# Optimization experiments

Measured on AMD Instinct MI355X. Metric: run time of the kernel, lower is better.

The kernel has to match this reference:

```python
import jax, jax.numpy as jnp
import numpy as np

B, S, HID = 2, 2048, 2048
NH, HD = 16, 128
KVC, QC = 512, 1536


def _rope(x):
    # x: [B, H, S, D]; interleaved-pair rotation matching the torch view(..., D//2, 2)
    b, h, s, d = x.shape
    inv_freq = 1.0 / (10000.0 ** (jnp.arange(0, d, 2, dtype=jnp.float32) / d))  # [D/2]
    pos = jnp.arange(s, dtype=jnp.float32)
    sinusoid = pos[:, None] * inv_freq[None, :]  # [S, D/2]
    sin = jnp.sin(sinusoid)[None, None]  # [1,1,S,D/2]
    cos = jnp.cos(sinusoid)[None, None]
    xr = x.reshape(b, h, s, d // 2, 2)
    x1, x2 = xr[..., 0], xr[..., 1]
    out = jnp.stack([x1 * cos - x2 * sin, x1 * sin + x2 * cos], axis=-1)
    return out.reshape(b, h, s, d)


def setup_inputs() -> dict:
    key = jax.random.key(0)
    ks = jax.random.split(key, 14)
    def lin(k, fan_in, fan_out):
        lim = 1.0 / np.sqrt(fan_in)
        kw, kb = jax.random.split(k)
        W = jax.random.uniform(kw, (fan_in, fan_out), jnp.float32, -lim, lim)
        b = jax.random.uniform(kb, (fan_out,), jnp.float32, -lim, lim)
        return W, b
    x = jax.random.normal(ks[0], (B, S, HID), jnp.float32)
    # causal mask (positions with 0 are masked out)
    attention_mask = jnp.tril(jnp.ones((S, S), jnp.int32))[None, None]  # [1,1,S,S]
    W_dkv, b_dkv = lin(ks[1], HID, KVC)
    W_uk, b_uk = lin(ks[2], KVC, NH * HD)
    W_uv, b_uv = lin(ks[3], KVC, NH * HD)
    W_dq, b_dq = lin(ks[4], HID, QC)
    W_uq, b_uq = lin(ks[5], QC, NH * HD)
    W_o, b_o = lin(ks[6], NH * HD, HID)
    return dict(x=x, attention_mask=attention_mask,
                W_dkv=W_dkv, b_dkv=b_dkv, W_uk=W_uk, b_uk=b_uk,
                W_uv=W_uv, b_uv=b_uv, W_dq=W_dq, b_dq=b_dq,
                W_uq=W_uq, b_uq=b_uq, W_o=W_o, b_o=b_o)


def reference(x, attention_mask, W_dkv, b_dkv, W_uk, b_uk, W_uv, b_uv,
              W_dq, b_dq, W_uq, b_uq, W_o, b_o):
    b, s, _ = x.shape
    kv = x @ W_dkv + b_dkv                                   # [B,S,KVC]
    k = (kv @ W_uk + b_uk).reshape(b, s, NH, HD).transpose(0, 2, 1, 3)  # [B,H,S,D]
    v = (kv @ W_uv + b_uv).reshape(b, s, NH, HD).transpose(0, 2, 1, 3)
    q = ((x @ W_dq + b_dq) @ W_uq + b_uq).reshape(b, s, NH, HD).transpose(0, 2, 1, 3)
    q, k = _rope(q), _rope(k)
    scores = jnp.einsum('bhqd,bhkd->bhqk', q, k) / jnp.sqrt(jnp.float32(HD))
    scores = jnp.where(attention_mask == 0, jnp.float32(-1e9), scores)
    probs = jax.nn.softmax(scores, axis=-1)
    out = jnp.einsum('bhqk,bhkd->bhqd', probs, v)            # [B,H,S,D]
    out = out.transpose(0, 2, 1, 3).reshape(b, s, NH * HD)
    return out @ W_o + b_o
```

## Files before the change

### kernel.cpp

```cpp
#include <hip/hip_runtime.h>
#include <stdint.h>

typedef unsigned short u16;
typedef uint32_t u32;
typedef __attribute__((ext_vector_type(8))) short short8;
typedef __attribute__((ext_vector_type(4))) float f32x4;
typedef __attribute__((ext_vector_type(4))) u32 u32x4;
typedef __attribute__((ext_vector_type(2))) u32 u32x2;
typedef __attribute__((ext_vector_type(4))) unsigned short u16x4;

#define BS_ 4096
#define S_ 2048
#define HID_ 2048

__device__ __forceinline__ float bf2f(u16 u) { union { u32 i; float f; } v; v.i = ((u32)u) << 16; return v.f; }
__device__ __forceinline__ u16 f2bf(float f) {
  union { float f; u32 i; } v; v.f = f;
  u32 r = v.i + 0x7fffu + ((v.i >> 16) & 1u);
  return (u16)(r >> 16);
}

__device__ __forceinline__ void gload16(const void* gsrc, void* ldst) {
  __builtin_amdgcn_global_load_lds(
      (const __attribute__((address_space(1))) void*)gsrc,
      (__attribute__((address_space(3))) void*)ldst, 16, 0, 0);
}

__global__ __launch_bounds__(256) void prep(const float* __restrict__ x, u16* __restrict__ xb,
                                            const float* __restrict__ W_dkv, const float* __restrict__ W_dq,
                                            const float* __restrict__ W_uk, const float* __restrict__ W_uv,
                                            const float* __restrict__ W_uq, const float* __restrict__ W_o,
                                            u16* __restrict__ WdkvqT, u16* __restrict__ WukvT,
                                            u16* __restrict__ WuqT, u16* __restrict__ WoT,
                                            const float* __restrict__ b_dkv, const float* __restrict__ b_dq,
                                            const float* __restrict__ b_uk, const float* __restrict__ b_uv,
                                            float* __restrict__ cs, float* __restrict__ bc1,
                                            float* __restrict__ bc2) {
  __shared__ float tile[64][65];
  int b = blockIdx.x;
  const int t = threadIdx.x;
  if (b < 8192) {
    int i = b * 256 + t;
    float4 v = ((const float4*)x)[i];
    u16x4 o;
    o.x = f2bf(v.x); o.y = f2bf(v.y); o.z = f2bf(v.z); o.w = f2bf(v.w);
    ((u16x4*)xb)[i] = o;
    return;
  }
  b -= 8192;
  if (b < 3328) {
    const float* W; u16* WT; int K, N, gx, r = b;
    if (r < 256)                 { W = W_dkv; WT = WdkvqT;                    K = 2048; N = 512;  gx = 8;  }
    else if ((r -= 256) < 768)   { W = W_dq;  WT = WdkvqT + (size_t)512 * 2048; K = 2048; N = 1536; gx = 24; }
    else if ((r -= 768) < 256)   { W = W_uk;  WT = WukvT;                     K = 512;  N = 2048; gx = 32; }
    else if ((r -= 256) < 256)   { W = W_uv;  WT = WukvT + (size_t)2048 * 512;  K = 512;  N = 2048; gx = 32; }
    else if ((r -= 256) < 768)   { W = W_uq;  WT = WuqT;                      K = 1536; N = 2048; gx = 32; }
    else                         { r -= 768;  W = W_o; WT = WoT;              K = 2048; N = 2048; gx = 32; }
    const int nb = (r % gx) * 64, kb = (r / gx) * 64;
#pragma unroll
    for (int c = 0; c < 4; ++c) {
      int idx = c * 256 + t;
      int row = idx >> 4;
      int col4 = (idx & 15) * 4;
      float4 v = *(const float4*)&W[(size_t)(kb + row) * N + nb + col4];
      tile[row][col4 + 0] = v.x; tile[row][col4 + 1] = v.y;
      tile[row][col4 + 2] = v.z; tile[row][col4 + 3] = v.w;
    }
    __syncthreads();
#pragma unroll
    for (int c = 0; c < 4; ++c) {
      int idx = c * 256 + t;
      int n = idx >> 4;
      int k4 = (idx & 15) * 4;
      u16x4 o;
      o.x = f2bf(tile[k4 + 0][n]); o.y = f2bf(tile[k4 + 1][n]);
      o.z = f2bf(tile[k4 + 2][n]); o.w = f2bf(tile[k4 + 3][n]);
      *(u16x4*)&WT[(size_t)(nb + n) * K + kb + k4] = o;
    }
    return;
  }
  b -= 3328;
  if (b < 512) {
    int idx = b * 256 + t;
    int pos = idx >> 6, i = idx & 63;
    float inv = powf(10000.f, -(float)i / 64.f);
    float a = (float)pos * inv;
    cs[idx * 2] = cosf(a);
    cs[idx * 2 + 1] = sinf(a);
    return;
  }
  b -= 512;
  {
    int i = b * 256 + t;
    if (i < 512) bc1[i] = b_dkv[i];
    else if (i < 2048) bc1[i] = b_dq[i - 512];
    else if (i < 4096) bc2[i - 2048] = b_uk[i - 2048];
    else if (i < 6144) bc2[i - 2048] = b_uv[i - 4096];
  }
}

template <int OUTF32>
__global__ __launch_bounds__(256) void gemm_bt(const u16* __restrict__ A, int lda,
                                               const u16* __restrict__ BT,
                                               const float* __restrict__ bias,
                                               void* __restrict__ Cout,
                                               int M, int N, int K) {
  __shared__ u16 As[2][128 * 64];
  __shared__ u16 Bs[2][128 * 64];
  const int t = threadIdx.x;
  const int lane = t & 63, wave = t >> 6;
  const int wm = wave >> 1, wn = wave & 1;
  const int gx = gridDim.x;
  const int nwg = gx * gridDim.y;
  const int flat = blockIdx.y * gx + blockIdx.x;
  const int swz = (flat & 7) * (nwg >> 3) + (flat >> 3);
  const int tn = swz % gx, tm = swz / gx;
  const int r16 = lane & 15, q4 = lane >> 4;

  f32x4 acc[4][4];
#pragma unroll
  for (int m = 0; m < 4; ++m)
#pragma unroll
    for (int n = 0; n < 4; ++n) acc[m][n] = (f32x4){0.f, 0.f, 0.f, 0.f};

  auto stg = [&](int bufi, int kt) {
#pragma unroll
    for (int c = 0; c < 4; ++c) {
      int idx = c * 256 + t;
      int row = idx >> 3, ch = idx & 7;
      gload16(&A[(size_t)(tm * 128 + row) * lda + kt + ch * 8], (char*)As[bufi] + idx * 16);
      gload16(&BT[(size_t)(tn * 128 + row) * K + kt + ch * 8], (char*)Bs[bufi] + idx * 16);
    }
  };

  const int nkt = K >> 6;
  stg(0, 0);
  __syncthreads();
  for (int it = 0; it < nkt; ++it) {
    const int buf = it & 1;
    if (it + 1 < nkt) stg(buf ^ 1, (it + 1) << 6);
#pragma unroll
    for (int kk = 0; kk < 64; kk += 32) {
      short8 af[4], bfv[4];
#pragma unroll
      for (int m = 0; m < 4; ++m)
        af[m] = *(const short8*)&As[buf][(wm * 64 + m * 16 + r16) * 64 + kk + q4 * 8];
#pragma unroll
      for (int n = 0; n < 4; ++n)
        bfv[n] = *(const short8*)&Bs[buf][(wn * 64 + n * 16 + r16) * 64 + kk + q4 * 8];
      __builtin_amdgcn_s_setprio(1);
#pragma unroll
      for (int m = 0; m < 4; ++m)
#pragma unroll
        for (int n = 0; n < 4; ++n)
          acc[m][n] = __builtin_amdgcn_mfma_f32_16x16x32_bf16(bfv[n], af[m], acc[m][n], 0, 0, 0);
      __builtin_amdgcn_s_setprio(0);
    }
    __syncthreads();
  }
#pragma unroll
  for (int n = 0; n < 4; ++n) {
    int gc0 = tn * 128 + wn * 64 + n * 16 + q4 * 4;
    float4 bv4 = *(const float4*)&bias[gc0];
#pragma unroll
    for (int m = 0; m < 4; ++m) {
      int grow = tm * 128 + wm * 64 + m * 16 + r16;
      float v0 = acc[m][n][0] + bv4.x, v1 = acc[m][n][1] + bv4.y;
      float v2 = acc[m][n][2] + bv4.z, v3 = acc[m][n][3] + bv4.w;
      if (OUTF32) {
        float4 o; o.x = v0; o.y = v1; o.z = v2; o.w = v3;
        *(float4*)&((float*)Cout)[(size_t)grow * N + gc0] = o;
      } else {
        u16x4 o; o.x = f2bf(v0); o.y = f2bf(v1); o.z = f2bf(v2); o.w = f2bf(v3);
        *(u16x4*)&((u16*)Cout)[(size_t)grow * N + gc0] = o;
      }
    }
  }
}

__global__ __launch_bounds__(256) void gemm23(const u16* __restrict__ kvq1,
                                              const u16* __restrict__ WukvT, const u16* __restrict__ WuqT,
                                              const float* __restrict__ bc2, const float* __restrict__ b_uq,
                                              const float* __restrict__ cs,
                                              u16* __restrict__ kbuf, u16* __restrict__ VT,
                                              u16* __restrict__ qb) {
  __shared__ u16 sh[2 * 128 * 64];
  u16* As = sh;
  u16* Bs = sh + 8192;
  const int t = threadIdx.x;
  const int lane = t & 63, wave = t >> 6;
  const int wm = wave >> 1, wn = wave & 1;
  const int bflat = blockIdx.x;
  const bool g2 = (bflat >= 512);
  const u16* A  = g2 ? kvq1 : (kvq1 + 512);
  const u16* BT = g2 ? WukvT : WuqT;
  const float* bias = g2 ? bc2 : b_uq;
  const int K = g2 ? 512 : 1536;
  const int gx = g2 ? 32 : 16;
  const int nwg = g2 ? 1024 : 512;
  const int flat = g2 ? (bflat - 512) : bflat;
  const int swz = (flat & 7) * (nwg >> 3) + (flat >> 3);
  const int tn = swz % gx, tm = swz / gx;
  const int r16 = lane & 15, q4 = lane >> 4;

  f32x4 acc[4][4];
#pragma unroll
  for (int m = 0; m < 4; ++m)
#pragma unroll
    for (int n = 0; n < 4; ++n) acc[m][n] = (f32x4){0.f, 0.f, 0.f, 0.f};

  for (int kt = 0; kt < K; kt += 64) {
#pragma unroll
    for (int c = 0; c < 4; ++c) {
      int idx = c * 256 + t;
      int row = idx >> 3, ch = idx & 7;
      gload16(&A[(size_t)(tm * 128 + row) * 2048 + kt + ch * 8], (char*)As + idx * 16);
      gload16(&BT[(size_t)(tn * 128 + row) * K + kt + ch * 8], (char*)Bs + idx * 16);
    }
    __syncthreads();
#pragma unroll
    for (int kk = 0; kk < 64; kk += 32) {
      short8 af[4], bfv[4];
#pragma unroll
      for (int m = 0; m < 4; ++m)
        af[m] = *(const short8*)&As[(wm * 64 + m * 16 + r16) * 64 + kk + q4 * 8];
#pragma unroll
      for (int n = 0; n < 4; ++n)
        bfv[n] = *(const short8*)&Bs[(wn * 64 + n * 16 + r16) * 64 + kk + q4 * 8];
      __builtin_amdgcn_s_setprio(1);
#pragma unroll
      for (int m = 0; m < 4; ++m)
#pragma unroll
        for (int n = 0; n < 4; ++n)
          acc[m][n] = __builtin_amdgcn_mfma_f32_16x16x32_bf16(bfv[n], af[m], acc[m][n], 0, 0, 0);
      __builtin_amdgcn_s_setprio(0);
    }
    __syncthreads();
  }

  const bool isV = g2 && (tn >= 16);
  if (!isV) {
    u16* outp = g2 ? kbuf : qb;
#pragma unroll
    for (int n = 0; n < 4; ++n) {
      int gc0 = tn * 128 + wn * 64 + n * 16 + q4 * 4;
      float4 bv4 = *(const float4*)&bias[gc0];
      const int i0 = (gc0 & 127) >> 1;
#pragma unroll
      for (int m = 0; m < 4; ++m) {
        int grow = tm * 128 + wm * 64 + m * 16 + r16;
        float v0 = acc[m][n][0] + bv4.x, v1 = acc[m][n][1] + bv4.y;
        float v2 = acc[m][n][2] + bv4.z, v3 = acc[m][n][3] + bv4.w;
        int s = grow & 2047;
        float4 cp = *(const float4*)&cs[((size_t)s * 64 + i0) * 2];
        float y0 = v0 * cp.x - v1 * cp.y;
        float y1 = v0 * cp.y + v1 * cp.x;
        float y2 = v2 * cp.z - v3 * cp.w;
        float y3 = v2 * cp.w + v3 * cp.z;
        u16x4 o; o.x = f2bf(y0); o.y = f2bf(y1); o.z = f2bf(y2); o.w = f2bf(y3);
        *(u16x4*)&outp[(size_t)grow * 2048 + gc0] = o;
      }
    }
  } else {
    u16* lt = sh;
#pragma unroll
    for (int n = 0; n < 4; ++n) {
      int gc0 = tn * 128 + wn * 64 + n * 16 + q4 * 4;
      float4 bv4 = *(const float4*)&bias[gc0];
      int dL0 = wn * 64 + n * 16 + q4 * 4;
#pragma unroll
      for (int m = 0; m < 4; ++m) {
        int sL = wm * 64 + m * 16 + r16;
        float vv[4] = {acc[m][n][0] + bv4.x, acc[m][n][1] + bv4.y,
                       acc[m][n][2] + bv4.z, acc[m][n][3] + bv4.w};
#pragma unroll
        for (int j = 0; j < 4; ++j) {
          int dd = dL0 + j;
          lt[dd * 128 + (sL ^ ((dd & 7) << 4))] = f2bf(vv[j]);
        }
      }
    }
    __syncthreads();
    const int hh = tn - 16;
    const int bb2 = tm >> 4;
    const int s0 = (tm & 15) * 128;
    u16* vbase = VT + (size_t)(bb2 * 16 + hh) * 128 * S_ + s0;
#pragma unroll
    for (int c = 0; c < 8; ++c) {
      int idx = c * 256 + t;
      int d = idx >> 4, ch = idx & 15;
      short8 v = *(const short8*)&lt[d * 128 + ((ch * 8) ^ ((d & 7) << 4))];
      *(short8*)&vbase[(size_t)d * S_ + ch * 8] = v;
    }
  }
}

__global__ __launch_bounds__(256, 2) void attn_kernel(const u16* __restrict__ Q, const u16* __restrict__ K,
                                                      int kld, const u16* __restrict__ VT,
                                                      u16* __restrict__ O) {
  __shared__ char smem[75776];
  u16* Kl = (u16*)smem;
  u16* Vl = (u16*)(smem + 32768);
  u16* Pl = (u16*)(smem + 65536);
  float* ex = (float*)smem;

  const int t = threadIdx.x;
  const int lane = t & 63, w = t >> 6;
  const int r16 = lane & 15, q4 = lane >> 4;
  const int par = w >> 1, sub = w & 1;
  const int b = blockIdx.x;
  const int xcd = b & 7, u = b >> 3;
  const int p = u & 15, g4 = u >> 4;
  const int bh = g4 * 8 + xcd;
  const int bb = bh >> 4, h = bh & 15;
  const u16* Qb = Q + (size_t)bb * S_ * HID_ + (size_t)h * 128;
  const u16* Kb = K + (size_t)bb * S_ * kld + (size_t)h * 128;
  const u16* VTb = VT + (size_t)bh * 128 * S_;
  u16* Ob = O + (size_t)bb * S_ * HID_ + (size_t)h * 128;

  auto stage = [&](int rs, int kvbase) {
#pragma unroll
    for (int pp = 0; pp < 2; ++pp) {
      int kvb = kvbase + pp * 32;
      char* kd = (char*)(Kl + (size_t)(rs * 2 + pp) * 4096);
      char* vd = (char*)(Vl + (size_t)(rs * 2 + pp) * 4096);
#pragma unroll
      for (int c = 0; c < 2; ++c) {
        int s = c * 256 + t;
        int row = s >> 4;
        int ch = (s & 15) ^ (row & 7);
        gload16(&Kb[(size_t)(kvb + row) * kld + ch * 8], kd + s * 16);
      }
#pragma unroll
      for (int c = 0; c < 2; ++c) {
        int s = c * 256 + t;
        int row = s >> 2;
        int ch = (s & 3) ^ ((row >> 1) & 3);
        gload16(&VTb[(size_t)row * S_ + kvb + ch * 8], vd + s * 16);
      }
    }
  };

  u16* Pw = Pl + (size_t)w * 1280;
  const float SCALE = 0.08838834764831845f;

#pragma unroll
  for (int seg = 0; seg < 2; ++seg) {
    const int qt = seg ? (31 - p) : p;
    const int nr = qt + 1;
    const int qrow0 = qt * 64 + sub * 32;

    short8 qf[2][4];
#pragma unroll
    for (int m = 0; m < 2; ++m)
#pragma unroll
      for (int dk = 0; dk < 4; ++dk)
        qf[m][dk] = *(const short8*)&Qb[(size_t)(qrow0 + m * 16 + r16) * HID_ + dk * 32 + q4 * 8];

    f32x4 ao[2][8];
    float mr[2], lr[2];
#pragma unroll
    for (int m = 0; m < 2; ++m) {
#pragma unroll
      for (int dn = 0; dn < 8; ++dn) ao[m][dn] = (f32x4){0.f, 0.f, 0.f, 0.f};
      mr[m] = -1e30f; lr[m] = 0.f;
    }

    stage(0, 0);
    __syncthreads();

    for (int r = 0; r < nr; ++r) {
      const int rs = r & 1;
      if (r + 1 < nr) stage(rs ^ 1, (r + 1) * 64);
      const int kv0 = r * 64 + par * 32;
      const u16* Kbuf = Kl + (size_t)(rs * 2 + par) * 4096;
      const u16* Vbuf = Vl + (size_t)(rs * 2 + par) * 4096;

      if (kv0 <= qrow0 + 31) {
        f32x4 sc[2][2];
#pragma unroll
        for (int m = 0; m < 2; ++m)
#pragma unroll
          for (int n = 0; n < 2; ++n) sc[m][n] = (f32x4){0.f, 0.f, 0.f, 0.f};
#pragma unroll
        for (int dk = 0; dk < 4; ++dk) {
          short8 kf[2];
#pragma unroll
          for (int n = 0; n < 2; ++n) {
            int kr = n * 16 + r16;
            int ba = (kr * 256 + dk * 64 + q4 * 16) ^ ((kr & 7) << 4);
            kf[n] = *(const short8*)((const char*)Kbuf + ba);
          }
          __builtin_amdgcn_s_setprio(1);
#pragma unroll
          for (int n = 0; n < 2; ++n)
#pragma unroll
            for (int m = 0; m < 2; ++m)
              sc[m][n] = __builtin_amdgcn_mfma_f32_16x16x32_bf16(kf[n], qf[m][dk], sc[m][n], 0, 0, 0);
          __builtin_amdgcn_s_setprio(0);
        }
        const bool nm = (kv0 + 31 > qrow0);
#pragma unroll
        for (int m = 0; m < 2; ++m) {
          const int q = qrow0 + m * 16 + r16;
#pragma unroll
          for (int n = 0; n < 2; ++n)
#pragma unroll
            for (int j = 0; j < 4; ++j) {
              float sv = sc[m][n][j] * SCALE;
              if (nm) {
                int kv = kv0 + n * 16 + q4 * 4 + j;
                if (kv > q) sv = -1e30f;
              }
              sc[m][n][j] = sv;
            }
        }
        float tm0[2];
#pragma unroll
        for (int m = 0; m < 2; ++m) {
          float tm = sc[m][0][0];
#pragma unroll
          for (int n = 0; n < 2; ++n)
#pragma unroll
            for (int j = 0; j < 4; ++j) tm = fmaxf(tm, sc[m][n][j]);
          tm = fmaxf(tm, __shfl_xor(tm, 16));
          tm = fmaxf(tm, __shfl_xor(tm, 32));
          tm0[m] = tm;
        }
        float growth = fmaxf(tm0[0] - mr[0], tm0[1] - mr[1]);
        if (!__all(growth <= 8.0f)) {
#pragma unroll
          for (int m = 0; m < 2; ++m) {
            float mnew = fmaxf(mr[m], tm0[m]);
            float fsc = __expf(mr[m] - mnew);
            lr[m] *= fsc; mr[m] = mnew;
#pragma unroll
            for (int dn = 0; dn < 8; ++dn) ao[m][dn] *= fsc;
          }
        }
#pragma unroll
        for (int m = 0; m < 2; ++m) {
          float ps = 0.f;
#pragma unroll
          for (int n = 0; n < 2; ++n)
#pragma unroll
            for (int j = 0; j < 4; ++j) {
              float pv = __expf(sc[m][n][j] - mr[m]);
              sc[m][n][j] = pv;
              ps += pv;
            }
          ps += __shfl_xor(ps, 16);
          ps += __shfl_xor(ps, 32);
          lr[m] += ps;
        }
#pragma unroll
        for (int m = 0; m < 2; ++m)
#pragma unroll
          for (int n = 0; n < 2; ++n) {
            u32 lo, hi;
            asm("v_cvt_pk_bf16_f32 %0, %1, %2" : "=v"(lo) : "v"(sc[m][n][0]), "v"(sc[m][n][1]));
            asm("v_cvt_pk_bf16_f32 %0, %1, %2" : "=v"(hi) : "v"(sc[m][n][2]), "v"(sc[m][n][3]));
            u32x2 pr; pr.x = lo; pr.y = hi;
            int ba = (m * 16 + r16) * 80 + n * 32 + q4 * 8;
            *(u32x2*)((char*)Pw + ba) = pr;
          }
        short8 pb[2];
#pragma unroll
        for (int m = 0; m < 2; ++m)
          pb[m] = *(const short8*)((const char*)Pw + (m * 16 + r16) * 80 + q4 * 16);
        __builtin_amdgcn_s_setprio(1);
#pragma unroll
        for (int dn = 0; dn < 8; ++dn) {
          int d = dn * 16 + r16;
          int bv = d * 64 + ((q4 ^ ((d >> 1) & 3)) * 16);
          short8 vf = *(const short8*)((const char*)Vbuf + bv);
#pragma unroll
          for (int m = 0; m < 2; ++m)
            ao[m][dn] = __builtin_amdgcn_mfma_f32_16x16x32_bf16(vf, pb[m], ao[m][dn], 0, 0, 0);
        }
        __builtin_amdgcn_s_setprio(0);
      }
      __syncthreads();
    }

    {
      float* exb = ex + (size_t)sub * 4352 + (size_t)lane * 68;
      if (par == 1) {
#pragma unroll
        for (int m = 0; m < 2; ++m)
#pragma unroll
          for (int dn = 0; dn < 8; ++dn)
            *(f32x4*)(exb + m * 32 + dn * 4) = ao[m][dn];
        exb[64] = mr[0]; exb[65] = mr[1]; exb[66] = lr[0]; exb[67] = lr[1];
      }
      __syncthreads();
      if (par == 0) {
#pragma unroll
        for (int m = 0; m < 2; ++m) {
          float mB = exb[64 + m], lB = exb[66 + m];
          float mx = fmaxf(mr[m], mB);
          float wA = __expf(mr[m] - mx), wB = __expf(mB - mx);
          float inv = 1.f / (lr[m] * wA + lB * wB);
          const int q = qrow0 + m * 16 + r16;
#pragma unroll
          for (int dn = 0; dn < 8; ++dn) {
            f32x4 ob = *(const f32x4*)(exb + m * 32 + dn * 4);
            u16x4 o;
#pragma unroll
            for (int j = 0; j < 4; ++j) o[j] = f2bf((ao[m][dn][j] * wA + ob[j] * wB) * inv);
            *(u16x4*)&Ob[(size_t)q * HID_ + dn * 16 + q4 * 4] = o;
          }
        }
      }
      __syncthreads();
    }
  }
}

extern "C" void kernel_launch(void* const* d_in, const int* in_sizes, int n_in,
                              void* d_out, int out_size, void* d_ws, size_t ws_size,
                              hipStream_t stream) {
  (void)in_sizes; (void)n_in; (void)out_size; (void)ws_size;
  const float* x     = (const float*)d_in[0];
  const float* W_dkv = (const float*)d_in[2];
  const float* b_dkv = (const float*)d_in[3];
  const float* W_uk  = (const float*)d_in[4];
  const float* b_uk  = (const float*)d_in[5];
  const float* W_uv  = (const float*)d_in[6];
  const float* b_uv  = (const float*)d_in[7];
  const float* W_dq  = (const float*)d_in[8];
  const float* b_dq  = (const float*)d_in[9];
  const float* W_uq  = (const float*)d_in[10];
  const float* b_uq  = (const float*)d_in[11];
  const float* W_o   = (const float*)d_in[12];
  const float* b_o   = (const float*)d_in[13];
  float* out = (float*)d_out;

  char* ws = (char*)d_ws;
  size_t off = 0;
  auto carve = [&](size_t bytes) { void* p = ws + off; off += (bytes + 255) & ~(size_t)255; return p; };
  u16* xb     = (u16*)carve((size_t)BS_ * 2048 * 2);
  u16* WdkvqT = (u16*)carve((size_t)2048 * 2048 * 2);
  u16* WukvT  = (u16*)carve((size_t)4096 * 512 * 2);
  u16* WuqT   = (u16*)carve((size_t)2048 * 1536 * 2);
  u16* WoT    = (u16*)carve((size_t)2048 * 2048 * 2);
  u16* kvq1   = (u16*)carve((size_t)BS_ * 2048 * 2);
  u16* kbuf   = (u16*)carve((size_t)BS_ * 2048 * 2);
  u16* qb     = (u16*)carve((size_t)BS_ * 2048 * 2);
  u16* aob    = (u16*)carve((size_t)BS_ * 2048 * 2);
  float* cs   = (float*)carve((size_t)2048 * 64 * 2 * 4);
  float* bc1  = (float*)carve((size_t)2048 * 4);
  float* bc2  = (float*)carve((size_t)4096 * 4);
  u16* VT     = xb;

  prep<<<dim3(12056), 256, 0, stream>>>(x, xb, W_dkv, W_dq, W_uk, W_uv, W_uq, W_o,
                                        WdkvqT, WukvT, WuqT, WoT,
                                        b_dkv, b_dq, b_uk, b_uv, cs, bc1, bc2);

  gemm_bt<0><<<dim3(2048 / 128, BS_ / 128), 256, 0, stream>>>(xb, 2048, WdkvqT, bc1, kvq1, BS_, 2048, 2048);

  gemm23<<<dim3(1536), 256, 0, stream>>>(kvq1, WukvT, WuqT, bc2, b_uq, cs, kbuf, VT, qb);

  attn_kernel<<<dim3(512), 256, 0, stream>>>(qb, kbuf, 2048, VT, aob);

  gemm_bt<1><<<dim3(2048 / 128, BS_ / 128), 256, 0, stream>>>(aob, 2048, WoT, b_o, out, BS_, 2048, 2048);
}
```

Baseline: 268.5 us.

## Double-buffer LDS tiles and interleave q/kv workgroups in gemm23

The q/kv up-projection kernel now keeps two LDS buffers and issues the global-to-LDS loads for the next K tile before computing on the current one, so memory latency overlaps with MFMA work. It also reorders the block-to-task mapping so every third workgroup runs the long-K q projection, interleaved with the short-K kv projection work, instead of putting all q work first. That should balance the load across CUs over time. The cost is doubling LDS use to 64KB, which may lower occupancy.

```diff
diff --git a/kernel.cpp b/kernel.cpp
--- a/kernel.cpp
+++ b/kernel.cpp
@@ -184,21 +184,19 @@
                                               const float* __restrict__ cs,
                                               u16* __restrict__ kbuf, u16* __restrict__ VT,
                                               u16* __restrict__ qb) {
-  __shared__ u16 sh[2 * 128 * 64];
-  u16* As = sh;
-  u16* Bs = sh + 8192;
+  __shared__ u16 sh[4 * 128 * 64];
   const int t = threadIdx.x;
   const int lane = t & 63, wave = t >> 6;
   const int wm = wave >> 1, wn = wave & 1;
   const int bflat = blockIdx.x;
-  const bool g2 = (bflat >= 512);
-  const u16* A  = g2 ? kvq1 : (kvq1 + 512);
-  const u16* BT = g2 ? WukvT : WuqT;
-  const float* bias = g2 ? bc2 : b_uq;
-  const int K = g2 ? 512 : 1536;
-  const int gx = g2 ? 32 : 16;
-  const int nwg = g2 ? 1024 : 512;
-  const int flat = g2 ? (bflat - 512) : bflat;
+  const bool g3 = (bflat % 3 == 0);
+  const u16* A  = g3 ? (kvq1 + 512) : kvq1;
+  const u16* BT = g3 ? WuqT : WukvT;
+  const float* bias = g3 ? b_uq : bc2;
+  const int K = g3 ? 1536 : 512;
+  const int gx = g3 ? 16 : 32;
+  const int nwg = g3 ? 512 : 1024;
+  const int flat = g3 ? (bflat / 3) : (bflat - bflat / 3 - 1);
   const int swz = (flat & 7) * (nwg >> 3) + (flat >> 3);
   const int tn = swz % gx, tm = swz / gx;
   const int r16 = lane & 15, q4 = lane >> 4;
@@ -209,15 +207,26 @@
 #pragma unroll
     for (int n = 0; n < 4; ++n) acc[m][n] = (f32x4){0.f, 0.f, 0.f, 0.f};
 
-  for (int kt = 0; kt < K; kt += 64) {
+  auto stg = [&](int bufi, int kt) {
+    char* Asb = (char*)(sh + bufi * 16384);
+    char* Bsb = Asb + 16384;
 #pragma unroll
     for (int c = 0; c < 4; ++c) {
       int idx = c * 256 + t;
       int row = idx >> 3, ch = idx & 7;
-      gload16(&A[(size_t)(tm * 128 + row) * 2048 + kt + ch * 8], (char*)As + idx * 16);
-      gload16(&BT[(size_t)(tn * 128 + row) * K + kt + ch * 8], (char*)Bs + idx * 16);
-    }
-    __syncthreads();
+      gload16(&A[(size_t)(tm * 128 + row) * 2048 + kt + ch * 8], Asb + idx * 16);
+      gload16(&BT[(size_t)(tn * 128 + row) * K + kt + ch * 8], Bsb + idx * 16);
+    }
+  };
+
+  const int nkt = K >> 6;
+  stg(0, 0);
+  __syncthreads();
+  for (int it = 0; it < nkt; ++it) {
+    const int buf = it & 1;
+    if (it + 1 < nkt) stg(buf ^ 1, (it + 1) << 6);
+    const u16* As = sh + buf * 16384;
+    const u16* Bs = As + 8192;
 #pragma unroll
     for (int kk = 0; kk < 64; kk += 32) {
       short8 af[4], bfv[4];
@@ -238,9 +247,9 @@
     __syncthreads();
   }
 
-  const bool isV = g2 && (tn >= 16);
+  const bool isV = (!g3) && (tn >= 16);
   if (!isV) {
-    u16* outp = g2 ? kbuf : qb;
+    u16* outp = g3 ? qb : kbuf;
 #pragma unroll
     for (int n = 0; n < 4; ++n) {
       int gc0 = tn * 128 + wn * 64 + n * 16 + q4 * 4;
```

Result: slower. 276.2 us (+2.8%).
